# Kernel tuning notes

Measured on AMD Instinct MI355X. Metric: run time of the kernel, lower is better.

Reference implementation:

```python
import jax, jax.numpy as jnp
import numpy as np

H = 16
D_MODEL = 1024
D_K = D_MODEL // H  # 64


def setup_inputs() -> dict:
    key = jax.random.key(0)
    ks = jax.random.split(key, 8)
    B, S = 8, 1024
    q = jax.random.normal(ks[0], (B, S, D_MODEL), dtype=jnp.float32)
    k = jax.random.normal(ks[1], (B, S, D_MODEL), dtype=jnp.float32)
    v = jax.random.normal(ks[2], (B, S, D_MODEL), dtype=jnp.float32)
    # xavier_normal for [h, d_model, d_k]: std = sqrt(2 / (d_model + d_k)) (fan over last two dims)
    std_p = float(np.sqrt(2.0 / (D_MODEL + D_K)))
    W_q = jax.random.normal(ks[3], (H, D_MODEL, D_K), dtype=jnp.float32) * std_p
    W_k = jax.random.normal(ks[4], (H, D_MODEL, D_K), dtype=jnp.float32) * std_p
    W_v = jax.random.normal(ks[5], (H, D_MODEL, D_K), dtype=jnp.float32) * std_p
    std_o = float(np.sqrt(2.0 / (H * D_K + D_MODEL)))
    W_o = jax.random.normal(ks[6], (D_MODEL, H * D_K), dtype=jnp.float32) * std_o  # torch Linear weight [out, in]
    b_o = jax.random.normal(ks[7], (D_MODEL,), dtype=jnp.float32) * 0.01
    return {"q": q, "k": k, "v": v, "W_q": W_q, "W_k": W_k, "W_v": W_v, "W_o": W_o, "b_o": b_o}


def reference(q, k, v, W_q, W_k, W_v, W_o, b_o):
    B, S, _ = q.shape
    # per-head projections: [h, b, s, d_k]
    qh = jnp.einsum('bsd,hdk->hbsk', q, W_q)
    kh = jnp.einsum('bsd,hdk->hbsk', k, W_k)
    vh = jnp.einsum('bsd,hdk->hbsk', v, W_v)
    scale = 1.0 / jnp.sqrt(jnp.asarray(D_K, dtype=q.dtype))
    scores = jnp.einsum('hbsk,hbtk->hbst', qh, kh) * scale  # [h,b,s,s]
    attn = jax.nn.softmax(scores, axis=-1)
    c = jnp.einsum('hbst,hbtk->hbsk', attn, vh)  # [h,b,s,d_k]
    # torch code splits the stacked (h*b) batch and concats on feature dim:
    # head index becomes the OUTER factor of the feature dim -> [b,s,h*d_k]
    c = jnp.transpose(c, (1, 2, 0, 3)).reshape(B, S, H * D_K)
    out = c @ W_o.T + b_o
    return out
```

## Files before the change

kernel.cpp:

```cpp
#include <hip/hip_runtime.h>
#include <hip/hip_bf16.h>

typedef __bf16 bf16_t;
typedef __attribute__((ext_vector_type(8))) __bf16 bf16x8;
typedef __attribute__((ext_vector_type(4))) float f32x4;

#define MFMA(a, b, c) __builtin_amdgcn_mfma_f32_16x16x32_bf16(a, b, c, 0, 0, 0)

__device__ inline void gload_lds16(const bf16_t* g, bf16_t* l) {
  __builtin_amdgcn_global_load_lds(
      (const __attribute__((address_space(1))) void*)g,
      (__attribute__((address_space(3))) void*)l, 16, 0, 0);
}

__global__ void fill_sentinel(float* out, int n, float val) {
  int i = blockIdx.x * blockDim.x + threadIdx.x;
  if (i < n) out[i] = val;
}

__global__ void transpose_w(const float* __restrict__ Wq, const float* __restrict__ Wk,
                            const float* __restrict__ Wv, bf16_t* __restrict__ Wt) {
  int gid = blockIdx.x * blockDim.x + threadIdx.x;
  int e = gid * 8;
  int m = e >> 20;
  int rem = e & 1048575;
  int n = rem >> 10;
  int d0 = rem & 1023;
  const float* W = (m == 0) ? Wq : (m == 1) ? Wk : Wv;
  int h = n >> 6, kk = n & 63;
  union { bf16_t h8[8]; uint4 u; } tmp;
#pragma unroll
  for (int j = 0; j < 8; ++j)
    tmp.h8[j] = (bf16_t)W[((size_t)(h * 1024 + d0 + j)) * 64 + kk];
  *(uint4*)(Wt + e) = tmp.u;
}

__global__ void cvt_bf16(const float* __restrict__ in, bf16_t* __restrict__ out) {
  size_t i = (size_t)(blockIdx.x * blockDim.x + threadIdx.x) * 8;
  f32x4 a = *(const f32x4*)(in + i);
  f32x4 b = *(const f32x4*)(in + i + 4);
  bf16x8 r;
  r[0] = (bf16_t)a[0]; r[1] = (bf16_t)a[1]; r[2] = (bf16_t)a[2]; r[3] = (bf16_t)a[3];
  r[4] = (bf16_t)b[0]; r[5] = (bf16_t)b[1]; r[6] = (bf16_t)b[2]; r[7] = (bf16_t)b[3];
  *(bf16x8*)(out + i) = r;
}

template <int MODE>
__global__ void gemm_bt(const bf16_t* __restrict__ A, const bf16_t* __restrict__ Bt,
                        const float* __restrict__ bias, void* __restrict__ out_,
                        int M, int N, int K) {
  __shared__ bf16_t sA[128 * 32];
  __shared__ bf16_t sB[128 * 32];
  const int t = threadIdx.x;
  const int w = t >> 6, l = t & 63;
  const int lq = l >> 4, ll = l & 15;
  const int m0 = blockIdx.x * 128, n0 = blockIdx.y * 128;
  const int wr = (w >> 1) * 64, wc = (w & 1) * 64;
  const int srow = l >> 2;
  const int scol = (l & 3) * 8;
  f32x4 acc[4][4] = {};
  for (int k0 = 0; k0 < K; k0 += 32) {
    __syncthreads();
#pragma unroll
    for (int c = 0; c < 2; ++c) {
      int ch = w * 2 + c;
      int row = ch * 16 + srow;
      gload_lds16(A  + (size_t)(m0 + row) * K + k0 + scol, sA + ch * 512);
      gload_lds16(Bt + (size_t)(n0 + row) * K + k0 + scol, sB + ch * 512);
    }
    __syncthreads();
    bf16x8 af[4], bfr[4];
#pragma unroll
    for (int i = 0; i < 4; ++i) {
      af[i]  = *(const bf16x8*)(sA + (wr + i * 16 + ll) * 32 + lq * 8);
      bfr[i] = *(const bf16x8*)(sB + (wc + i * 16 + ll) * 32 + lq * 8);
    }
#pragma unroll
    for (int mi = 0; mi < 4; ++mi)
#pragma unroll
      for (int ni = 0; ni < 4; ++ni)
        acc[mi][ni] = MFMA(af[mi], bfr[ni], acc[mi][ni]);
  }
#pragma unroll
  for (int mi = 0; mi < 4; ++mi)
#pragma unroll
    for (int ni = 0; ni < 4; ++ni)
#pragma unroll
      for (int r = 0; r < 4; ++r) {
        int row = m0 + wr + mi * 16 + lq * 4 + r;
        int col = n0 + wc + ni * 16 + ll;
        float v = acc[mi][ni][r];
        if (MODE == 2) {
          ((float*)out_)[(size_t)row * N + col] = v + bias[col];
        } else {
          int h = col >> 6, kk = col & 63, b = row >> 10, s = row & 1023;
          size_t idx;
          if (MODE == 0)
            idx = ((size_t)((h * 8 + b) * 1024 + s)) * 64 + kk;
          else
            idx = ((size_t)((h * 8 + b) * 64 + kk)) * 1024 + s;
          ((bf16_t*)out_)[idx] = (bf16_t)v;
        }
      }
}

__global__ void attn_kernel(const bf16_t* __restrict__ qh, const bf16_t* __restrict__ kh,
                            const bf16_t* __restrict__ vt, bf16_t* __restrict__ c) {
  constexpr int QP = 72, KP = 72, VP = 136, PP = 136;
  __shared__ bf16_t sQ[64 * QP];
  __shared__ bf16_t sK[128 * KP];
  __shared__ bf16_t sV[64 * VP];
  __shared__ bf16_t sP[4][16 * PP];
  const int t = threadIdx.x;
  const int w = t >> 6, l = t & 63;
  const int lq = l >> 4, ll = l & 15;
  const int q0 = blockIdx.x * 64;
  const int hb = blockIdx.y;
  const int h = hb >> 3, b = hb & 7;
  const size_t base = (size_t)hb * 65536;
  const bf16_t* Q = qh + base + (size_t)q0 * 64;
  const bf16_t* K = kh + base;
  const bf16_t* V = vt + base;
#pragma unroll
  for (int r = 0; r < 2; ++r) {
    int e = (r * 256 + t) * 8;
    int row = e >> 6, col = e & 63;
    *(uint4*)(sQ + row * QP + col) = *(const uint4*)(Q + e);
  }
  float mrow[4], lrow[4];
  f32x4 o[4] = {};
#pragma unroll
  for (int r = 0; r < 4; ++r) { mrow[r] = -1e30f; lrow[r] = 0.f; }

  for (int kt = 0; kt < 1024; kt += 128) {
    __syncthreads();
#pragma unroll
    for (int r = 0; r < 4; ++r) {
      int e = (r * 256 + t) * 8;
      int row = e >> 6, col = e & 63;
      *(uint4*)(sK + row * KP + col) = *(const uint4*)(K + (size_t)kt * 64 + e);
      int rowv = e >> 7, colv = e & 127;
      *(uint4*)(sV + rowv * VP + colv) =
          *(const uint4*)(V + (size_t)rowv * 1024 + kt + colv);
    }
    __syncthreads();
    f32x4 sacc[8] = {};
    bf16x8 aq[2];
#pragma unroll
    for (int ks = 0; ks < 2; ++ks)
      aq[ks] = *(const bf16x8*)(sQ + (w * 16 + ll) * QP + ks * 32 + lq * 8);
#pragma unroll
    for (int ni = 0; ni < 8; ++ni)
#pragma unroll
      for (int ks = 0; ks < 2; ++ks) {
        bf16x8 bk = *(const bf16x8*)(sK + (ni * 16 + ll) * KP + ks * 32 + lq * 8);
        sacc[ni] = MFMA(aq[ks], bk, sacc[ni]);
      }
    float rmax[4] = {-1e30f, -1e30f, -1e30f, -1e30f};
#pragma unroll
    for (int ni = 0; ni < 8; ++ni)
#pragma unroll
      for (int r = 0; r < 4; ++r) {
        sacc[ni][r] *= 0.125f;
        rmax[r] = fmaxf(rmax[r], sacc[ni][r]);
      }
#pragma unroll
    for (int off = 1; off < 16; off <<= 1)
#pragma unroll
      for (int r = 0; r < 4; ++r)
        rmax[r] = fmaxf(rmax[r], __shfl_xor(rmax[r], off));
    float alpha[4];
#pragma unroll
    for (int r = 0; r < 4; ++r) {
      float mnew = fmaxf(mrow[r], rmax[r]);
      alpha[r] = __expf(mrow[r] - mnew);
      mrow[r] = mnew;
    }
    float rs[4] = {0.f, 0.f, 0.f, 0.f};
#pragma unroll
    for (int ni = 0; ni < 8; ++ni)
#pragma unroll
      for (int r = 0; r < 4; ++r) {
        float p = __expf(sacc[ni][r] - mrow[r]);
        sacc[ni][r] = p;
        rs[r] += p;
      }
#pragma unroll
    for (int off = 1; off < 16; off <<= 1)
#pragma unroll
      for (int r = 0; r < 4; ++r)
        rs[r] += __shfl_xor(rs[r], off);
#pragma unroll
    for (int r = 0; r < 4; ++r)
      lrow[r] = lrow[r] * alpha[r] + rs[r];
#pragma unroll
    for (int ni = 0; ni < 4; ++ni)
#pragma unroll
      for (int r = 0; r < 4; ++r)
        o[ni][r] *= alpha[r];
    bf16_t* Pw = sP[w];
#pragma unroll
    for (int ni = 0; ni < 8; ++ni)
#pragma unroll
      for (int r = 0; r < 4; ++r)
        Pw[(lq * 4 + r) * PP + ni * 16 + ll] = (bf16_t)sacc[ni][r];
    asm volatile("s_waitcnt lgkmcnt(0)" ::: "memory");
#pragma unroll
    for (int ks = 0; ks < 4; ++ks) {
      bf16x8 ap = *(const bf16x8*)(Pw + ll * PP + ks * 32 + lq * 8);
#pragma unroll
      for (int ni = 0; ni < 4; ++ni) {
        bf16x8 bv = *(const bf16x8*)(sV + (ni * 16 + ll) * VP + ks * 32 + lq * 8);
        o[ni] = MFMA(ap, bv, o[ni]);
      }
    }
  }
#pragma unroll
  for (int ni = 0; ni < 4; ++ni)
#pragma unroll
    for (int r = 0; r < 4; ++r) {
      int s = q0 + w * 16 + lq * 4 + r;
      int dk = ni * 16 + ll;
      float val = o[ni][r] / lrow[r];
      c[((size_t)(b * 1024 + s)) * 1024 + h * 64 + dk] = (bf16_t)val;
    }
}

extern "C" void kernel_launch(void* const* d_in, const int* in_sizes, int n_in,
                              void* d_out, int out_size, void* d_ws, size_t ws_size,
                              hipStream_t stream) {
  float* out = (float*)d_out;
  int nblk_out = (out_size + 255) / 256;
  if (n_in != 8) {
    fill_sentinel<<<nblk_out, 256, 0, stream>>>(out, out_size, 600.0f + 10.0f * n_in);
    return;
  }
  const int expect[8] = {8388608, 8388608, 8388608, 1048576,
                         1048576, 1048576, 1048576, 1024};
  for (int i = 0; i < 8; ++i)
    if (in_sizes[i] != expect[i]) {
      fill_sentinel<<<nblk_out, 256, 0, stream>>>(out, out_size, 500.0f + 10.0f * i);
      return;
    }

  bf16_t* ws   = (bf16_t*)d_ws;
  bf16_t* qhb  = ws;
  bf16_t* khb  = ws + 8388608;
  bf16_t* vtb  = ws + 16777216;
  bf16_t* Wt   = ws + 25165824;
  bf16_t* cbuf = ws + 25165824;
  bf16_t* Wob  = ws;
  if (ws_size < 67108864ull) {
    fill_sentinel<<<nblk_out, 256, 0, stream>>>(out, out_size, 400.0f);
    return;
  }

  const float* q  = (const float*)d_in[0];
  const float* k  = (const float*)d_in[1];
  const float* v  = (const float*)d_in[2];
  const float* Wq = (const float*)d_in[3];
  const float* Wk = (const float*)d_in[4];
  const float* Wv = (const float*)d_in[5];
  const float* Wo = (const float*)d_in[6];
  const float* bo = (const float*)d_in[7];

  bf16_t* qb = (bf16_t*)d_out;
  bf16_t* kb = (bf16_t*)d_out + 8388608;
  bf16_t* vb = (bf16_t*)d_out;

  transpose_w<<<1536, 256, 0, stream>>>(Wq, Wk, Wv, Wt);
  cvt_bf16<<<4096, 256, 0, stream>>>(q, qb);
  cvt_bf16<<<4096, 256, 0, stream>>>(k, kb);
  dim3 gg(64, 8);
  gemm_bt<0><<<gg, 256, 0, stream>>>(qb, Wt,           nullptr, qhb, 8192, 1024, 1024);
  gemm_bt<0><<<gg, 256, 0, stream>>>(kb, Wt + 1048576, nullptr, khb, 8192, 1024, 1024);
  cvt_bf16<<<4096, 256, 0, stream>>>(v, vb);
  gemm_bt<1><<<gg, 256, 0, stream>>>(vb, Wt + 2097152, nullptr, vtb, 8192, 1024, 1024);
  attn_kernel<<<dim3(16, 128), 256, 0, stream>>>(qhb, khb, vtb, cbuf);
  cvt_bf16<<<512, 256, 0, stream>>>(Wo, Wob);
  gemm_bt<2><<<gg, 256, 0, stream>>>(cbuf, Wob, bo, out, 8192, 1024, 1024);
}
```

Before: 438.2 us.

## Fold softmax scale into Q projection, lazy rescale, stream V from global

Folds the 1/sqrt(d_k) scale into the Q projection epilogue and shrinks the attention key tile from 128 to 64. V is no longer staged in LDS; the P·V MFMA operands are read directly from global memory. The online-softmax rescale becomes lazy: the running max and the output/sum rescale are updated only when some row's tile max exceeds the stored max by more than 8 (checked with a wave vote). This removes LDS traffic and a barrier's worth of staging plus most exp/multiply rescale work, at the cost of uncoalesced-ish global V reads and twice as many loop iterations and barriers.

```diff
diff --git a/kernel.cpp b/kernel.cpp
--- a/kernel.cpp
+++ b/kernel.cpp
@@ -48,7 +48,7 @@
 template <int MODE>
 __global__ void gemm_bt(const bf16_t* __restrict__ A, const bf16_t* __restrict__ Bt,
                         const float* __restrict__ bias, void* __restrict__ out_,
-                        int M, int N, int K) {
+                        int M, int N, int K, float scale) {
   __shared__ bf16_t sA[128 * 32];
   __shared__ bf16_t sB[128 * 32];
   const int t = threadIdx.x;
@@ -99,17 +99,16 @@
             idx = ((size_t)((h * 8 + b) * 1024 + s)) * 64 + kk;
           else
             idx = ((size_t)((h * 8 + b) * 64 + kk)) * 1024 + s;
-          ((bf16_t*)out_)[idx] = (bf16_t)v;
+          ((bf16_t*)out_)[idx] = (bf16_t)(v * scale);
         }
       }
 }
 
 __global__ void attn_kernel(const bf16_t* __restrict__ qh, const bf16_t* __restrict__ kh,
                             const bf16_t* __restrict__ vt, bf16_t* __restrict__ c) {
-  constexpr int QP = 72, KP = 72, VP = 136, PP = 136;
+  constexpr int QP = 72, KP = 72, PP = 72;
   __shared__ bf16_t sQ[64 * QP];
-  __shared__ bf16_t sK[128 * KP];
-  __shared__ bf16_t sV[64 * VP];
+  __shared__ bf16_t sK[64 * KP];
   __shared__ bf16_t sP[4][16 * PP];
   const int t = threadIdx.x;
   const int w = t >> 6, l = t & 63;
@@ -132,25 +131,22 @@
 #pragma unroll
   for (int r = 0; r < 4; ++r) { mrow[r] = -1e30f; lrow[r] = 0.f; }
 
-  for (int kt = 0; kt < 1024; kt += 128) {
-    __syncthreads();
-#pragma unroll
-    for (int r = 0; r < 4; ++r) {
+  for (int kt = 0; kt < 1024; kt += 64) {
+    __syncthreads();
+#pragma unroll
+    for (int r = 0; r < 2; ++r) {
       int e = (r * 256 + t) * 8;
       int row = e >> 6, col = e & 63;
       *(uint4*)(sK + row * KP + col) = *(const uint4*)(K + (size_t)kt * 64 + e);
-      int rowv = e >> 7, colv = e & 127;
-      *(uint4*)(sV + rowv * VP + colv) =
-          *(const uint4*)(V + (size_t)rowv * 1024 + kt + colv);
-    }
-    __syncthreads();
-    f32x4 sacc[8] = {};
+    }
+    __syncthreads();
+    f32x4 sacc[4] = {};
     bf16x8 aq[2];
 #pragma unroll
     for (int ks = 0; ks < 2; ++ks)
       aq[ks] = *(const bf16x8*)(sQ + (w * 16 + ll) * QP + ks * 32 + lq * 8);
 #pragma unroll
-    for (int ni = 0; ni < 8; ++ni)
+    for (int ni = 0; ni < 4; ++ni)
 #pragma unroll
       for (int ks = 0; ks < 2; ++ks) {
         bf16x8 bk = *(const bf16x8*)(sK + (ni * 16 + ll) * KP + ks * 32 + lq * 8);
@@ -158,27 +154,34 @@
       }
     float rmax[4] = {-1e30f, -1e30f, -1e30f, -1e30f};
 #pragma unroll
-    for (int ni = 0; ni < 8; ++ni)
+    for (int ni = 0; ni < 4; ++ni)
+#pragma unroll
+      for (int r = 0; r < 4; ++r)
+        rmax[r] = fmaxf(rmax[r], sacc[ni][r]);
+#pragma unroll
+    for (int off = 1; off < 16; off <<= 1)
+#pragma unroll
+      for (int r = 0; r < 4; ++r)
+        rmax[r] = fmaxf(rmax[r], __shfl_xor(rmax[r], off));
+    bool ok = true;
+#pragma unroll
+    for (int r = 0; r < 4; ++r)
+      ok = ok && (rmax[r] <= mrow[r] + 8.0f);
+    if (!__all(ok)) {
 #pragma unroll
       for (int r = 0; r < 4; ++r) {
-        sacc[ni][r] *= 0.125f;
-        rmax[r] = fmaxf(rmax[r], sacc[ni][r]);
-      }
-#pragma unroll
-    for (int off = 1; off < 16; off <<= 1)
-#pragma unroll
-      for (int r = 0; r < 4; ++r)
-        rmax[r] = fmaxf(rmax[r], __shfl_xor(rmax[r], off));
-    float alpha[4];
-#pragma unroll
-    for (int r = 0; r < 4; ++r) {
-      float mnew = fmaxf(mrow[r], rmax[r]);
-      alpha[r] = __expf(mrow[r] - mnew);
-      mrow[r] = mnew;
+        float mnew = fmaxf(mrow[r], rmax[r]);
+        float alpha = __expf(mrow[r] - mnew);
+        mrow[r] = mnew;
+        lrow[r] *= alpha;
+#pragma unroll
+        for (int ni = 0; ni < 4; ++ni)
+          o[ni][r] *= alpha;
+      }
     }
     float rs[4] = {0.f, 0.f, 0.f, 0.f};
 #pragma unroll
-    for (int ni = 0; ni < 8; ++ni)
+    for (int ni = 0; ni < 4; ++ni)
 #pragma unroll
       for (int r = 0; r < 4; ++r) {
         float p = __expf(sacc[ni][r] - mrow[r]);
@@ -192,25 +195,20 @@
         rs[r] += __shfl_xor(rs[r], off);
 #pragma unroll
     for (int r = 0; r < 4; ++r)
-      lrow[r] = lrow[r] * alpha[r] + rs[r];
-#pragma unroll
-    for (int ni = 0; ni < 4; ++ni)
-#pragma unroll
-      for (int r = 0; r < 4; ++r)
-        o[ni][r] *= alpha[r];
+      lrow[r] += rs[r];
     bf16_t* Pw = sP[w];
 #pragma unroll
-    for (int ni = 0; ni < 8; ++ni)
+    for (int ni = 0; ni < 4; ++ni)
 #pragma unroll
       for (int r = 0; r < 4; ++r)
         Pw[(lq * 4 + r) * PP + ni * 16 + ll] = (bf16_t)sacc[ni][r];
     asm volatile("s_waitcnt lgkmcnt(0)" ::: "memory");
 #pragma unroll
-    for (int ks = 0; ks < 4; ++ks) {
+    for (int ks = 0; ks < 2; ++ks) {
       bf16x8 ap = *(const bf16x8*)(Pw + ll * PP + ks * 32 + lq * 8);
 #pragma unroll
       for (int ni = 0; ni < 4; ++ni) {
-        bf16x8 bv = *(const bf16x8*)(sV + (ni * 16 + ll) * VP + ks * 32 + lq * 8);
+        bf16x8 bv = *(const bf16x8*)(V + (size_t)(ni * 16 + ll) * 1024 + kt + ks * 32 + lq * 8);
         o[ni] = MFMA(ap, bv, o[ni]);
       }
     }
@@ -272,11 +270,11 @@
   cvt_bf16<<<4096, 256, 0, stream>>>(q, qb);
   cvt_bf16<<<4096, 256, 0, stream>>>(k, kb);
   dim3 gg(64, 8);
-  gemm_bt<0><<<gg, 256, 0, stream>>>(qb, Wt,           nullptr, qhb, 8192, 1024, 1024);
-  gemm_bt<0><<<gg, 256, 0, stream>>>(kb, Wt + 1048576, nullptr, khb, 8192, 1024, 1024);
+  gemm_bt<0><<<gg, 256, 0, stream>>>(qb, Wt,           nullptr, qhb, 8192, 1024, 1024, 0.125f);
+  gemm_bt<0><<<gg, 256, 0, stream>>>(kb, Wt + 1048576, nullptr, khb, 8192, 1024, 1024, 1.0f);
   cvt_bf16<<<4096, 256, 0, stream>>>(v, vb);
-  gemm_bt<1><<<gg, 256, 0, stream>>>(vb, Wt + 2097152, nullptr, vtb, 8192, 1024, 1024);
+  gemm_bt<1><<<gg, 256, 0, stream>>>(vb, Wt + 2097152, nullptr, vtb, 8192, 1024, 1024, 1.0f);
   attn_kernel<<<dim3(16, 128), 256, 0, stream>>>(qhb, khb, vtb, cbuf);
   cvt_bf16<<<512, 256, 0, stream>>>(Wo, Wob);
-  gemm_bt<2><<<gg, 256, 0, stream>>>(cbuf, Wob, bo, out, 8192, 1024, 1024);
-}
+  gemm_bt<2><<<gg, 256, 0, stream>>>(cbuf, Wob, bo, out, 8192, 1024, 1024, 1.0f);
+}
```

Measured after the change: 431.4 us. About the same (-1.5%).
